# Kernel tuning notes

Hardware: AMD Instinct MI355X
Metric: run time of the kernel (lower is better)

Reference implementation:

```python
import jax, jax.numpy as jnp
import numpy as np

RADIUS = 0.15
NSAMPLE = 128
NPOINT = 128
EPS = 1e-5  # BatchNorm eps (eval mode, running_mean=0, running_var=1)


def _bn(x, g, b):
    shape = (1, -1) + (1,) * (x.ndim - 2)
    return x * (g / jnp.sqrt(1.0 + EPS)).reshape(shape) + b.reshape(shape)


def _fps(x, npoint):
    # farthest point sampling; x: (Bk, N, 3) -> (Bk, npoint) int32
    Bn, N, _ = x.shape

    def step(carry, _):
        dist, far = carry
        c = jnp.take_along_axis(x, far[:, None, None], 1)  # (Bk,1,3)
        d = jnp.sum((x - c) ** 2, -1)
        dist = jnp.minimum(dist, d)
        return (dist, jnp.argmax(dist, -1).astype(jnp.int32)), far

    init = (jnp.full((Bn, N), 1e10, x.dtype), jnp.zeros((Bn,), jnp.int32))
    _, idxs = jax.lax.scan(step, init, None, length=npoint)
    return idxs.T  # (Bk, npoint)


def _sa_module(x, f, mlp):
    # PointnetSAModuleVotes: FPS -> ball query -> group (use_xyz, normalize_xyz)
    # -> shared MLP (conv2d 1x1 + BN + ReLU) -> max over nsample.
    Bk, M, _ = x.shape
    fps_idx = _fps(x, NPOINT)
    new_xyz = jnp.take_along_axis(x, fps_idx[..., None], 1)  # (Bk,np,3)
    d2 = jnp.sum((new_xyz[:, :, None, :] - x[:, None, :, :]) ** 2, -1)  # (Bk,np,M)
    cand = jnp.where(d2 < RADIUS ** 2, jnp.arange(M)[None, None, :], M)
    cand = jnp.sort(cand, -1)[..., :NSAMPLE]  # first nsample in-radius indices
    first = cand[..., :1]
    first = jnp.where(first == M, 0, first)
    idx = jnp.where(cand == M, first, cand)  # (Bk,np,ns), pad with first valid
    gx = jnp.take_along_axis(x, idx.reshape(Bk, -1)[..., None], 1).reshape(Bk, NPOINT, NSAMPLE, 3)
    gxn = (gx - new_xyz[:, :, None, :]) / RADIUS  # normalize_xyz=True
    gf = jnp.take_along_axis(f[:, :, None, :], idx[:, None, :, :], 3)  # (Bk,C,np,ns)
    h = jnp.concatenate([gxn.transpose(0, 3, 1, 2), gf], 1)  # (Bk, C+3, np, ns)
    for (w, b, g, be) in mlp:
        h = jax.nn.relu(_bn(jnp.einsum('oc,bcps->bops', w, h) + b[None, :, None, None], g, be))
    return new_xyz, h.max(-1)  # (Bk,np,3), (Bk,128,np)


def setup_inputs() -> dict:
    key = jax.random.key(0)
    ks = iter(jax.random.split(key, 40))
    B, M, K, C = 2, 1024, 19, 256
    inp = {}
    inp['xyz'] = jax.random.normal(next(ks), (B, M, K, 3), jnp.float32)
    inp['features'] = jax.random.normal(next(ks), (B, C, K, M), jnp.float32)

    def conv_p(prefix, cin, cout):
        inp[prefix + '_w'] = jax.random.normal(next(ks), (cout, cin), jnp.float32) * (1.0 / np.sqrt(cin))
        inp[prefix + '_b'] = jax.random.normal(next(ks), (cout,), jnp.float32) * 0.02
        inp[prefix + '_g'] = 1.0 + 0.1 * jax.random.normal(next(ks), (cout,), jnp.float32)
        inp[prefix + '_be'] = 0.02 * jax.random.normal(next(ks), (cout,), jnp.float32)

    conv_p('m1', C + 3, 128)  # use_xyz -> 259 in-channels
    conv_p('m2', 128, 128)
    conv_p('m3', 128, 128)
    conv_p('c1', 128, 128)
    conv_p('c2', 128, 128)
    inp['op_w'] = jax.random.normal(next(ks), (K, 5, 128), jnp.float32) * (1.0 / np.sqrt(128))
    inp['op_b'] = jax.random.normal(next(ks), (K, 5), jnp.float32) * 0.02
    return inp


def reference(xyz, features, m1_w, m1_b, m1_g, m1_be, m2_w, m2_b, m2_g, m2_be,
              m3_w, m3_b, m3_g, m3_be, c1_w, c1_b, c1_g, c1_be,
              c2_w, c2_b, c2_g, c2_be, op_w, op_b):
    B, M, K, _ = xyz.shape
    C = features.shape[1]
    # fold vote_factor k into the batch dim (all per-k SA/conv weights are shared)
    x = xyz.transpose(0, 2, 1, 3).reshape(B * K, M, 3)
    f = features.transpose(0, 2, 1, 3).reshape(B * K, C, M)
    mlp = [(m1_w, m1_b, m1_g, m1_be), (m2_w, m2_b, m2_g, m2_be), (m3_w, m3_b, m3_g, m3_be)]
    new_xyz, feat = _sa_module(x, f, mlp)
    net = jax.nn.relu(_bn(jnp.einsum('oc,bcp->bop', c1_w, feat) + c1_b[None, :, None], c1_g, c1_be))
    net = jax.nn.relu(_bn(jnp.einsum('oc,bcp->bop', c2_w, net) + c2_b[None, :, None], c2_g, c2_be))
    net = net.reshape(B, K, 128, NPOINT)
    # per-k output conv (conv_op ModuleList), 128 -> 2+3
    out = jnp.einsum('koc,bkcp->bkop', op_w, net) + op_b[None, :, :, None]
    net_t = out.transpose(0, 1, 3, 2)  # (B,K,np,5)
    agg_xyz = new_xyz.reshape(B, K, NPOINT, 3)
    center = agg_xyz + net_t[..., 2:5]  # decode_scores_
    scores = jnp.concatenate([net_t[..., :2], center], -1)  # obj(2) + center(3)
    return scores, agg_xyz, feat.reshape(B, K, 128, NPOINT)
```

## Files before the change

kernel.cpp:

```cpp
#include <hip/hip_runtime.h>
#include <math.h>

#define NBK   38

#define OFF_XC    0u
#define OFF_NXYZ  466944u
#define OFF_BIDX  525312u
#define OFF_W1F   3015680u
#define OFF_PREP  22938624u
#define OFF_WF    22955008u
#define OFF_CNT   23348224u

#define OUT_AGG   24320
#define OUT_FEAT  38912

typedef short bf16x8 __attribute__((ext_vector_type(8)));
typedef float f32x4  __attribute__((ext_vector_type(4)));
typedef int   v4i    __attribute__((ext_vector_type(4)));
typedef int   v2i    __attribute__((ext_vector_type(2)));

__device__ __forceinline__ float dist2f(float a0, float a1, float a2,
                                        float b0, float b1, float b2) {
#pragma clang fp contract(off)
  float d0 = a0 - b0;
  float d1 = a1 - b1;
  float d2 = a2 - b2;
  return d0 * d0 + d1 * d1 + d2 * d2;
}

__device__ __forceinline__ void split2rn(float v, unsigned& sh, unsigned& sm) {
  unsigned u = __float_as_uint(v);
  unsigned rh = (u + 0x7fffu + ((u >> 16) & 1u)) & 0xffff0000u;
  sh = rh >> 16;
  float r1 = v - __uint_as_float(rh);
  unsigned u1 = __float_as_uint(r1);
  unsigned rm = (u1 + 0x7fffu + ((u1 >> 16) & 1u)) & 0xffff0000u;
  sm = rm >> 16;
}

#define DPP_FMAX_STEP(v, ctrl)                                                 \
  {                                                                            \
    int _s = __builtin_amdgcn_update_dpp(__float_as_int(v), __float_as_int(v), \
                                         (ctrl), 0xf, 0xf, false);             \
    (v) = fmaxf((v), __int_as_float(_s));                                      \
  }

__device__ __forceinline__ float readlane_f(float v, int l) {
  return __int_as_float(__builtin_amdgcn_readlane(__float_as_int(v), l));
}

__global__ __launch_bounds__(512, 2) void front_kernel(
    const float* __restrict__ xyz, const float* __restrict__ feats,
    const float* __restrict__ m1w, const float* __restrict__ m1b,
    const float* __restrict__ m1g, const float* __restrict__ m1be,
    const float* __restrict__ m2w, const float* __restrict__ m2b,
    const float* __restrict__ m2g, const float* __restrict__ m2be,
    const float* __restrict__ m3w, const float* __restrict__ m3b,
    const float* __restrict__ m3g, const float* __restrict__ m3be,
    const float* __restrict__ c1w, const float* __restrict__ c1b,
    const float* __restrict__ c1g, const float* __restrict__ c1be,
    const float* __restrict__ c2w, const float* __restrict__ c2b,
    const float* __restrict__ c2g, const float* __restrict__ c2be,
    float* __restrict__ xc, float* __restrict__ nxyz, float* __restrict__ agg,
    int* __restrict__ bidx, int* __restrict__ counts,
    float* __restrict__ W1f, short* __restrict__ Wf, float* __restrict__ prep)
{
  __shared__ __align__(16) char smem[32768];
  int bid = blockIdx.x, t = threadIdx.x;
  int wave = t >> 6, lane = t & 63;

  if (bid < NBK) {
    int bk = bid;
    int b = bk / 19, k = bk % 19;
    float4* sp4 = (float4*)smem;
    float4* scen4 = (float4*)(smem + 16384);
    int* sfar = (int*)(smem + 18432);
    int2* cexch = (int2*)(smem + 18944);

    for (int i = t; i < 1024; i += 512) {
      const float* src = xyz + ((size_t)((b * 1024 + i) * 19 + k)) * 3;
      float x0 = src[0], x1 = src[1], x2 = src[2];
      sp4[i] = make_float4(x0, x1, x2, 0.f);
      xc[(bk * 3 + 0) * 1024 + i] = x0;
      xc[(bk * 3 + 1) * 1024 + i] = x1;
      xc[(bk * 3 + 2) * 1024 + i] = x2;
    }
    if (t == 0) sfar[0] = 0;
    __syncthreads();

    float px[8], py[8], pz[8], dist[8];
    if (wave < 2) {
      __builtin_amdgcn_s_setprio(1);
      int mbase = (wave << 9) + (lane << 3);
#pragma unroll
      for (int j = 0; j < 8; ++j) {
        float4 p = sp4[mbase + j];
        px[j] = p.x; py[j] = p.y; pz[j] = p.z;
        dist[j] = 1e10f;
      }
    }

    int far = 0;
    for (int it = 1; it < 128; ++it) {
      if (wave < 2) {
        float4 c = sp4[far];
#pragma unroll
        for (int j = 0; j < 8; ++j) {
          float d = dist2f(px[j], py[j], pz[j], c.x, c.y, c.z);
          dist[j] = fminf(dist[j], d);
        }
        float tv[4]; int tj[4];
#pragma unroll
        for (int i = 0; i < 4; ++i) {
          bool L = dist[2 * i] >= dist[2 * i + 1];
          tv[i] = L ? dist[2 * i] : dist[2 * i + 1];
          tj[i] = L ? (2 * i) : (2 * i + 1);
        }
        {
          bool L0 = tv[0] >= tv[1];
          float v0 = L0 ? tv[0] : tv[1]; int j0 = L0 ? tj[0] : tj[1];
          bool L1 = tv[2] >= tv[3];
          float v1 = L1 ? tv[2] : tv[3]; int j1 = L1 ? tj[2] : tj[3];
          bool L = v0 >= v1;
          tv[0] = L ? v0 : v1; tj[0] = L ? j0 : j1;
        }
        float lmax = tv[0];
        float g = lmax;
        DPP_FMAX_STEP(g, 0x111);
        DPP_FMAX_STEP(g, 0x112);
        DPP_FMAX_STEP(g, 0x114);
        DPP_FMAX_STEP(g, 0x118);
        float r0 = readlane_f(g, 15);
        float r1 = readlane_f(g, 31);
        float r2 = readlane_f(g, 47);
        float r3 = readlane_f(g, 63);
        float gmax = fmaxf(fmaxf(r0, r1), fmaxf(r2, r3));
        unsigned long long mk = __ballot(lmax == gmax);
        int wl = (int)__builtin_ctzll(mk);
        int lj = (lane << 3) + tj[0];
        int cand_m = (wave << 9) + __builtin_amdgcn_readlane(lj, wl);
        if (lane == 0) cexch[(it & 1) * 2 + wave] =
            make_int2(__float_as_int(gmax), cand_m);
      }
      __syncthreads();
      if (wave < 2) {
        int2 c0 = cexch[(it & 1) * 2 + 0];
        int2 c1 = cexch[(it & 1) * 2 + 1];
        far = (__int_as_float(c1.x) > __int_as_float(c0.x)) ? c1.y : c0.y;
        if (t == 0) sfar[it] = far;
      }
    }
    if (wave < 2) __builtin_amdgcn_s_setprio(0);
    __syncthreads();

    if (t < 128) {
      float4 c = sp4[sfar[t]];
      scen4[t] = c;
      nxyz[bk * 384 + t * 3 + 0] = c.x;
      nxyz[bk * 384 + t * 3 + 1] = c.y;
      nxyz[bk * 384 + t * 3 + 2] = c.z;
      agg[bk * 384 + t * 3 + 0] = c.x;
      agg[bk * 384 + t * 3 + 1] = c.y;
      agg[bk * 384 + t * 3 + 2] = c.z;
    }
    __syncthreads();

    for (int p = wave * 16; p < wave * 16 + 16; ++p) {
      float4 cen = scen4[p];
      int* outp = bidx + ((size_t)(bk * 128 + p)) * 128;
      int count = 0, first = 0;
      bool got = false;
      for (int ch = 0; ch < 16 && count < 128; ++ch) {
        int m = (ch << 6) + lane;
        float4 pv = sp4[m];
        float d = dist2f(pv.x, pv.y, pv.z, cen.x, cen.y, cen.z);
        bool flag = d < 0.0225f;
        unsigned long long mask = __ballot(flag);
        if (!got && mask) { first = (ch << 6) + __builtin_ctzll(mask); got = true; }
        int pos = count + (int)__popcll(mask & ((1ull << lane) - 1ull));
        if (flag && pos < 128) outp[pos] = m;
        count += (int)__popcll(mask);
      }
      for (int j = count + lane; j < 128; j += 64) outp[j] = first;
      if (lane == 0) counts[bk * 128 + p] = count > 128 ? 128 : count;
    }
    return;
  }

  if (bid < 342) {
    short* ffrag = (short*)smem;
    if (t >= 256) {
      for (int i = 0; i < 8; ++i) __syncthreads();
      return;
    }
    int blk = bid - NBK;
    int bk = blk >> 3, m0 = (blk & 7) << 7;
    int b = bk / 19, k = bk % 19;
    int quad = lane >> 4, nl = lane & 15;
    int mloc = t & 127, chalf = t >> 7;
    int st_w = mloc >> 4, sl_w = mloc & 15;
    const float* fbase = feats + ((size_t)(b * 4864 + k)) * 1024 + m0 + mloc;

    f32x4 acc[2][8];
#pragma unroll
    for (int oi = 0; oi < 2; ++oi)
#pragma unroll
      for (int st = 0; st < 8; ++st) acc[oi][st] = (f32x4){0.f, 0.f, 0.f, 0.f};

    for (int ch = 0; ch < 4; ++ch) {
      int cbase = ch * 64 + chalf * 32;
#pragma unroll
      for (int g = 0; g < 4; ++g) {
        float v[8];
#pragma unroll
        for (int j = 0; j < 8; ++j)
          v[j] = fbase[(size_t)(cbase + g * 8 + j) * 19456];
        unsigned sh[8], sm[8];
#pragma unroll
        for (int j = 0; j < 8; ++j) split2rn(v[j], sh[j], sm[j]);
        int base = chalf * 4096 + st_w * 512 + (g * 16 + sl_w) * 8;
        v4i ph = {(int)(sh[0] | (sh[1] << 16)), (int)(sh[2] | (sh[3] << 16)),
                  (int)(sh[4] | (sh[5] << 16)), (int)(sh[6] | (sh[7] << 16))};
        *(v4i*)&ffrag[base] = ph;
        v4i pm = {(int)(sm[0] | (sm[1] << 16)), (int)(sm[2] | (sm[3] << 16)),
                  (int)(sm[4] | (sm[5] << 16)), (int)(sm[6] | (sm[7] << 16))};
        *(v4i*)&ffrag[base + 8192] = pm;
      }
      __syncthreads();
#pragma unroll
      for (int kkl = 0; kkl < 2; ++kkl) {
        int kk = ch * 2 + kkl;
        bf16x8 a[2][2];
#pragma unroll
        for (int oi = 0; oi < 2; ++oi) {
          int o_row = (wave * 2 + oi) * 16 + nl;
          const float* wsrc = m1w + o_row * 259 + 3 + kk * 32 + quad * 8;
          float wv[8];
#pragma unroll
          for (int j = 0; j < 8; ++j) wv[j] = wsrc[j];
          unsigned sh[8], sm[8];
#pragma unroll
          for (int j = 0; j < 8; ++j) split2rn(wv[j], sh[j], sm[j]);
          short ah[8], am[8];
#pragma unroll
          for (int j = 0; j < 8; ++j) { ah[j] = (short)sh[j]; am[j] = (short)sm[j]; }
          a[oi][0] = (bf16x8){ah[0], ah[1], ah[2], ah[3], ah[4], ah[5], ah[6], ah[7]};
          a[oi][1] = (bf16x8){am[0], am[1], am[2], am[3], am[4], am[5], am[6], am[7]};
        }
#pragma unroll
        for (int st = 0; st < 8; ++st) {
          const short* hb = ffrag + kkl * 4096 + st * 512 + lane * 8;
          bf16x8 b0 = *(const bf16x8*)hb;
          bf16x8 b1 = *(const bf16x8*)(hb + 8192);
#pragma unroll
          for (int oi = 0; oi < 2; ++oi) {
            f32x4 c = acc[oi][st];
            c = __builtin_amdgcn_mfma_f32_16x16x32_bf16(a[oi][1], b0, c, 0, 0, 0);
            c = __builtin_amdgcn_mfma_f32_16x16x32_bf16(a[oi][0], b1, c, 0, 0, 0);
            c = __builtin_amdgcn_mfma_f32_16x16x32_bf16(a[oi][0], b0, c, 0, 0, 0);
            acc[oi][st] = c;
          }
        }
      }
      __syncthreads();
    }
    float inv = 1.0f / sqrtf(1.0f + 1e-5f);
#pragma unroll
    for (int oi = 0; oi < 2; ++oi) {
      int o0 = (wave * 2 + oi) * 16 + quad * 4;
      float4 bb = *(const float4*)&m1b[o0];
      float4 gg = *(const float4*)&m1g[o0];
#pragma unroll
      for (int st = 0; st < 8; ++st) {
        int m_out = m0 + st * 16 + nl;
        f32x4 cc = acc[oi][st];
        float4 r;
        r.x = (cc[0] + bb.x) * (gg.x * inv);
        r.y = (cc[1] + bb.y) * (gg.y * inv);
        r.z = (cc[2] + bb.z) * (gg.z * inv);
        r.w = (cc[3] + bb.w) * (gg.w * inv);
        *(float4*)&W1f[((size_t)(bk * 1024 + m_out)) * 128 + o0] = r;
      }
    }
    return;
  }

  if (bid < 358) {
    int idx = (bid - 342) * 512 + t;
#pragma unroll
    for (int e = 0; e < 4; ++e) {
      int i = idx * 4 + e;
      int c = i & 127, o = (i >> 7) & 127, l = i >> 14;
      float w = (l ? m3w : m2w)[o * 128 + c];
      unsigned sh, sm;
      split2rn(w, sh, sm);
      int ot = o >> 4, mm = o & 15, kk = c >> 5, q = (c & 31) >> 3, j = c & 7;
      int within = (q * 16 + mm) * 8 + j;
      Wf[(((l * 2 + 0) * 4 + kk) * 8 + ot) * 512 + within] = (short)sh;
      Wf[(((l * 2 + 1) * 4 + kk) * 8 + ot) * 512 + within] = (short)sm;
    }
    return;
  }

  if (bid < 374) {
    int idx2 = (bid - 358) * 512 + t;
#pragma unroll
    for (int e = 0; e < 4; ++e) {
      int i = idx2 * 4 + e;
      int c = i & 127, o = (i >> 7) & 127, l = i >> 14;
      float w = (l ? c2w : c1w)[o * 128 + c];
      unsigned sh, sm;
      split2rn(w, sh, sm);
      int ot = o >> 4, mm = o & 15, kk = c >> 5, q = (c & 31) >> 3, j = c & 7;
      int within = (q * 16 + mm) * 8 + j;
      Wf[131072 + (((l * 2 + 0) * 4 + kk) * 8 + ot) * 512 + within] = (short)sh;
      Wf[131072 + (((l * 2 + 1) * 4 + kk) * 8 + ot) * 512 + within] = (short)sm;
    }
    return;
  }

  if (t < 128) {
    float inv = 1.0f / sqrtf(1.0f + 1e-5f);
    float a1 = m1g[t] * inv;
    prep[t] = a1;
    float a2 = m2g[t] * inv;  prep[256 + t] = a2;  prep[384 + t] = fmaf(m2b[t], a2, m2be[t]);
    float a3 = m3g[t] * inv;  prep[512 + t] = a3;  prep[640 + t] = fmaf(m3b[t], a3, m3be[t]);
    float ac1 = c1g[t] * inv; prep[768 + t] = ac1; prep[896 + t] = fmaf(c1b[t], ac1, c1be[t]);
    float ac2 = c2g[t] * inv; prep[1024 + t] = ac2; prep[1152 + t] = fmaf(c2b[t], ac2, c2be[t]);
    prep[1280 + 4 * t + 0] = m1w[t * 259 + 0] * a1;
    prep[1280 + 4 * t + 1] = m1w[t * 259 + 1] * a1;
    prep[1280 + 4 * t + 2] = m1w[t * 259 + 2] * a1;
    prep[1280 + 4 * t + 3] = m1be[t];
  }
}

__device__ __forceinline__ void mfma_layer(const short* __restrict__ Wf,
                                           const short* hfrag, int l,
                                           int wave, int lane, int nst_h,
                                           f32x4 acc[2][4])
{
#pragma unroll 1
  for (int kk = 0; kk < 4; ++kk) {
    bf16x8 a[2][2];
#pragma unroll
    for (int oi = 0; oi < 2; ++oi)
#pragma unroll
      for (int sp = 0; sp < 2; ++sp)
        a[oi][sp] = *(const bf16x8*)(Wf + (((l * 2 + sp) * 4 + kk) * 8 + (wave * 2 + oi)) * 512 + lane * 8);
    for (int st = 0; st < nst_h; ++st) {
      const short* hb = hfrag + kk * 2048 + st * 512 + lane * 8;
      bf16x8 b0 = *(const bf16x8*)(hb);
      bf16x8 b1 = *(const bf16x8*)(hb + 8192);
#pragma unroll
      for (int oi = 0; oi < 2; ++oi) {
        f32x4 c = acc[oi][st];
        c = __builtin_amdgcn_mfma_f32_16x16x32_bf16(a[oi][1], b0, c, 0, 0, 0);
        c = __builtin_amdgcn_mfma_f32_16x16x32_bf16(a[oi][0], b1, c, 0, 0, 0);
        c = __builtin_amdgcn_mfma_f32_16x16x32_bf16(a[oi][0], b0, c, 0, 0, 0);
        acc[oi][st] = c;
      }
    }
  }
}

__global__ __launch_bounds__(256, 3) void sa_kernel(
    const float* __restrict__ xc, const float* __restrict__ nxyz,
    const int* __restrict__ bidx, const int* __restrict__ counts,
    const float* __restrict__ W1f, const float* __restrict__ prep,
    const short* __restrict__ Wf, float* __restrict__ feat_out)
{
  __shared__ __align__(16) short hfrag[16384];
  __shared__ float pcs[512];
  __shared__ float sm[32 * 128];
  __shared__ float ccen[12];
  __shared__ int scnt[4];
  int gb = blockIdx.x, bk = gb >> 5, pb = (gb & 31) << 2;
  int t = threadIdx.x;
  int wave = t >> 6, lane = t & 63;
  int quad = lane >> 4, nl = lane & 15;

  pcs[t] = prep[1280 + t];
  pcs[256 + t] = prep[1536 + t];
  if (t < 4) scnt[t] = counts[bk * 128 + pb + t];
  if (t < 12) {
    int bb = t / 3, c = t % 3;
    ccen[t] = nxyz[(bk * 128 + pb + bb) * 3 + c];
  }
  __syncthreads();
  int n0 = (scnt[0] + 15) >> 4, n1 = (scnt[1] + 15) >> 4;
  int n2 = (scnt[2] + 15) >> 4, n3 = (scnt[3] + 15) >> 4;
  int pf1 = n0, pf2 = n0 + n1, pf3 = n0 + n1 + n2, T = n0 + n1 + n2 + n3;

  for (int q0 = 0; q0 < T; q0 += 4) {
    int nst_h = T - q0;
    if (nst_h > 4) nst_h = 4;
    {
      int cg = wave;
      int st = lane >> 4, sl = lane & 15;
      if (st < nst_h) {
        int q = q0 + st;
        int bq = (q >= pf1) + (q >= pf2) + (q >= pf3);
        int tstart = (bq == 0) ? 0 : (bq == 1) ? pf1 : (bq == 2) ? pf2 : pf3;
        int tslot = q - tstart;
        int m = bidx[((size_t)(bk * 128 + pb + bq)) * 128 + tslot * 16 + sl];
        float cen0 = ccen[bq * 3 + 0], cen1 = ccen[bq * 3 + 1], cen2 = ccen[bq * 3 + 2];
        float g0 = (xc[(bk * 3 + 0) * 1024 + m] - cen0) * (1.0f / 0.15f);
        float g1 = (xc[(bk * 3 + 1) * 1024 + m] - cen1) * (1.0f / 0.15f);
        float g2 = (xc[(bk * 3 + 2) * 1024 + m] - cen2) * (1.0f / 0.15f);
        const float4* wrow = (const float4*)(W1f + ((size_t)(bk * 1024 + m)) * 128 + cg * 32);
        const float4* pcp = (const float4*)pcs + cg * 32;
#pragma unroll
        for (int g = 0; g < 4; ++g) {
          float4 wva = wrow[g * 2], wvb = wrow[g * 2 + 1];
          float wv[8] = {wva.x, wva.y, wva.z, wva.w, wvb.x, wvb.y, wvb.z, wvb.w};
          unsigned sh[8], smv[8];
#pragma unroll
          for (int e = 0; e < 8; ++e) {
            float4 pc = pcp[g * 8 + e];
            float hv = fmaxf(wv[e] + pc.x * g0 + pc.y * g1 + pc.z * g2 + pc.w, 0.f);
            split2rn(hv, sh[e], smv[e]);
          }
          int base = (cg * 4 + st) * 512 + (g * 16 + sl) * 8;
          v4i ph = {(int)(sh[0] | (sh[1] << 16)), (int)(sh[2] | (sh[3] << 16)),
                    (int)(sh[4] | (sh[5] << 16)), (int)(sh[6] | (sh[7] << 16))};
          *(v4i*)&hfrag[base] = ph;
          v4i pm = {(int)(smv[0] | (smv[1] << 16)), (int)(smv[2] | (smv[3] << 16)),
                    (int)(smv[4] | (smv[5] << 16)), (int)(smv[6] | (smv[7] << 16))};
          *(v4i*)&hfrag[base + 8192] = pm;
        }
      }
    }
    __syncthreads();

    f32x4 acc[2][4];
#pragma unroll
    for (int oi = 0; oi < 2; ++oi)
#pragma unroll
      for (int st = 0; st < 4; ++st) acc[oi][st] = (f32x4){0.f, 0.f, 0.f, 0.f};
    mfma_layer(Wf, hfrag, 0, wave, lane, nst_h, acc);
    __syncthreads();

#pragma unroll
    for (int oi = 0; oi < 2; ++oi) {
      int o0 = (wave * 2 + oi) * 16 + quad * 4;
      float4 al = *(const float4*)&prep[256 + o0];
      float4 be = *(const float4*)&prep[384 + o0];
      int kk2 = o0 >> 5, g2 = (o0 & 31) >> 3, j0 = o0 & 7;
      for (int st = 0; st < nst_h; ++st) {
        f32x4 cc = acc[oi][st];
        float v0 = fmaxf(fmaf(cc[0], al.x, be.x), 0.f);
        float v1 = fmaxf(fmaf(cc[1], al.y, be.y), 0.f);
        float v2 = fmaxf(fmaf(cc[2], al.z, be.z), 0.f);
        float v3 = fmaxf(fmaf(cc[3], al.w, be.w), 0.f);
        unsigned h0, m0_, h1, m1_, h2, m2_, h3, m3_;
        split2rn(v0, h0, m0_); split2rn(v1, h1, m1_);
        split2rn(v2, h2, m2_); split2rn(v3, h3, m3_);
        int base = (kk2 * 4 + st) * 512 + (g2 * 16 + nl) * 8 + j0;
        v2i w0 = {(int)(h0 | (h1 << 16)), (int)(h2 | (h3 << 16))};
        *(v2i*)&hfrag[base] = w0;
        v2i w1 = {(int)(m0_ | (m1_ << 16)), (int)(m2_ | (m3_ << 16))};
        *(v2i*)&hfrag[base + 8192] = w1;
      }
    }
    __syncthreads();

#pragma unroll
    for (int oi = 0; oi < 2; ++oi)
#pragma unroll
      for (int st = 0; st < 4; ++st) acc[oi][st] = (f32x4){0.f, 0.f, 0.f, 0.f};
    mfma_layer(Wf, hfrag, 1, wave, lane, nst_h, acc);

#pragma unroll
    for (int oi = 0; oi < 2; ++oi) {
      int o0 = (wave * 2 + oi) * 16 + quad * 4;
      float4 al = *(const float4*)&prep[512 + o0];
      float4 be = *(const float4*)&prep[640 + o0];
      for (int st = 0; st < nst_h; ++st) {
        f32x4 cc = acc[oi][st];
        float v[4];
        v[0] = fmaxf(fmaf(cc[0], al.x, be.x), 0.f);
        v[1] = fmaxf(fmaf(cc[1], al.y, be.y), 0.f);
        v[2] = fmaxf(fmaf(cc[2], al.z, be.z), 0.f);
        v[3] = fmaxf(fmaf(cc[3], al.w, be.w), 0.f);
#pragma unroll
        for (int r = 0; r < 4; ++r) {
          float x = v[r];
          x = fmaxf(x, __shfl_xor(x, 1));
          x = fmaxf(x, __shfl_xor(x, 2));
          x = fmaxf(x, __shfl_xor(x, 4));
          x = fmaxf(x, __shfl_xor(x, 8));
          if (nl == 0) sm[(q0 + st) * 128 + o0 + r] = x;
        }
      }
    }
    __syncthreads();
  }

#pragma unroll
  for (int e = t; e < 512; e += 256) {
    int bb = e >> 7, o = e & 127;
    int qs = (bb == 0) ? 0 : (bb == 1) ? pf1 : (bb == 2) ? pf2 : pf3;
    int nq = (bb == 0) ? n0 : (bb == 1) ? n1 : (bb == 2) ? n2 : n3;
    float v = sm[qs * 128 + o];
    for (int q = 1; q < nq; ++q) v = fmaxf(v, sm[(qs + q) * 128 + o]);
    feat_out[(((size_t)bk) << 14) + (o << 7) + pb + bb] = v;
  }
}

__global__ __launch_bounds__(256) void head_kernel(const float* __restrict__ featg,
    const float* __restrict__ prep, const short* __restrict__ Wf,
    const float* __restrict__ nxyz, const float* __restrict__ opw,
    const float* __restrict__ opb, float* __restrict__ scores)
{
  __shared__ __align__(16) short hfrag[16384];
  __shared__ float hplain[128 * 65];
  int bk = blockIdx.x >> 1, p0 = (blockIdx.x & 1) << 6;
  int t = threadIdx.x;
  int wave = t >> 6, lane = t & 63;
  int quad = lane >> 4, nl = lane & 15;
  const short* WC = Wf + 131072;

  {
    int cg = wave;
    int st = lane >> 4, sl = lane & 15;
    const float* fb = featg + (bk << 14) + p0 + lane;
#pragma unroll
    for (int g = 0; g < 4; ++g) {
      float v[8];
#pragma unroll
      for (int e = 0; e < 8; ++e)
        v[e] = fb[(cg * 32 + g * 8 + e) << 7];
      unsigned sh[8], sm[8];
#pragma unroll
      for (int e = 0; e < 8; ++e) split2rn(v[e], sh[e], sm[e]);
      int base = (cg * 4 + st) * 512 + (g * 16 + sl) * 8;
      v4i ph = {(int)(sh[0] | (sh[1] << 16)), (int)(sh[2] | (sh[3] << 16)),
                (int)(sh[4] | (sh[5] << 16)), (int)(sh[6] | (sh[7] << 16))};
      *(v4i*)&hfrag[base] = ph;
      v4i pm = {(int)(sm[0] | (sm[1] << 16)), (int)(sm[2] | (sm[3] << 16)),
                (int)(sm[4] | (sm[5] << 16)), (int)(sm[6] | (sm[7] << 16))};
      *(v4i*)&hfrag[base + 8192] = pm;
    }
  }
  __syncthreads();

  f32x4 acc[2][4];
#pragma unroll
  for (int oi = 0; oi < 2; ++oi)
#pragma unroll
    for (int st = 0; st < 4; ++st) acc[oi][st] = (f32x4){0.f, 0.f, 0.f, 0.f};
  mfma_layer(WC, hfrag, 0, wave, lane, 4, acc);
  __syncthreads();

#pragma unroll
  for (int oi = 0; oi < 2; ++oi) {
    int o0 = (wave * 2 + oi) * 16 + quad * 4;
    float4 al = *(const float4*)&prep[768 + o0];
    float4 be = *(const float4*)&prep[896 + o0];
    int kk2 = o0 >> 5, g2 = (o0 & 31) >> 3, j0 = o0 & 7;
#pragma unroll
    for (int st = 0; st < 4; ++st) {
      f32x4 cc = acc[oi][st];
      float v0 = fmaxf(fmaf(cc[0], al.x, be.x), 0.f);
      float v1 = fmaxf(fmaf(cc[1], al.y, be.y), 0.f);
      float v2 = fmaxf(fmaf(cc[2], al.z, be.z), 0.f);
      float v3 = fmaxf(fmaf(cc[3], al.w, be.w), 0.f);
      unsigned h0, m0_, h1, m1_, h2, m2_, h3, m3_;
      split2rn(v0, h0, m0_); split2rn(v1, h1, m1_);
      split2rn(v2, h2, m2_); split2rn(v3, h3, m3_);
      int base = (kk2 * 4 + st) * 512 + (g2 * 16 + nl) * 8 + j0;
      v2i w0 = {(int)(h0 | (h1 << 16)), (int)(h2 | (h3 << 16))};
      *(v2i*)&hfrag[base] = w0;
      v2i w1 = {(int)(m0_ | (m1_ << 16)), (int)(m2_ | (m3_ << 16))};
      *(v2i*)&hfrag[base + 8192] = w1;
    }
  }
  __syncthreads();

#pragma unroll
  for (int oi = 0; oi < 2; ++oi)
#pragma unroll
    for (int st = 0; st < 4; ++st) acc[oi][st] = (f32x4){0.f, 0.f, 0.f, 0.f};
  mfma_layer(WC, hfrag, 1, wave, lane, 4, acc);

#pragma unroll
  for (int oi = 0; oi < 2; ++oi) {
    int o0 = (wave * 2 + oi) * 16 + quad * 4;
    float4 al = *(const float4*)&prep[1024 + o0];
    float4 be = *(const float4*)&prep[1152 + o0];
#pragma unroll
    for (int st = 0; st < 4; ++st) {
      f32x4 cc = acc[oi][st];
      int p = st * 16 + nl;
      hplain[(o0 + 0) * 65 + p] = fmaxf(fmaf(cc[0], al.x, be.x), 0.f);
      hplain[(o0 + 1) * 65 + p] = fmaxf(fmaf(cc[1], al.y, be.y), 0.f);
      hplain[(o0 + 2) * 65 + p] = fmaxf(fmaf(cc[2], al.z, be.z), 0.f);
      hplain[(o0 + 3) * 65 + p] = fmaxf(fmaf(cc[3], al.w, be.w), 0.f);
    }
  }
  __syncthreads();

  if (t < 64) {
    int p = t, k = bk % 19;
    float res[5];
#pragma unroll
    for (int j = 0; j < 5; ++j) {
      const float* wr = opw + ((size_t)(k * 5 + j)) * 128;
      float a = opb[k * 5 + j];
      for (int c = 0; c < 128; ++c) a = fmaf(wr[c], hplain[c * 65 + p], a);
      res[j] = a;
    }
    int pg = p0 + p;
    float a0 = nxyz[(bk * 128 + pg) * 3 + 0];
    float a1 = nxyz[(bk * 128 + pg) * 3 + 1];
    float a2 = nxyz[(bk * 128 + pg) * 3 + 2];
    float* sc = scores + ((size_t)(bk * 128 + pg)) * 5;
    sc[0] = res[0];
    sc[1] = res[1];
    sc[2] = a0 + res[2];
    sc[3] = a1 + res[3];
    sc[4] = a2 + res[4];
  }
}

extern "C" void kernel_launch(void* const* d_in, const int* in_sizes, int n_in,
                              void* d_out, int out_size, void* d_ws, size_t ws_size,
                              hipStream_t stream) {
  (void)in_sizes; (void)n_in; (void)out_size; (void)ws_size;
  const float* xyz  = (const float*)d_in[0];
  const float* fts  = (const float*)d_in[1];
  const float* m1w  = (const float*)d_in[2];
  const float* m1b  = (const float*)d_in[3];
  const float* m1g  = (const float*)d_in[4];
  const float* m1be = (const float*)d_in[5];
  const float* m2w  = (const float*)d_in[6];
  const float* m2b  = (const float*)d_in[7];
  const float* m2g  = (const float*)d_in[8];
  const float* m2be = (const float*)d_in[9];
  const float* m3w  = (const float*)d_in[10];
  const float* m3b  = (const float*)d_in[11];
  const float* m3g  = (const float*)d_in[12];
  const float* m3be = (const float*)d_in[13];
  const float* c1w  = (const float*)d_in[14];
  const float* c1b  = (const float*)d_in[15];
  const float* c1g  = (const float*)d_in[16];
  const float* c1be = (const float*)d_in[17];
  const float* c2w  = (const float*)d_in[18];
  const float* c2b  = (const float*)d_in[19];
  const float* c2g  = (const float*)d_in[20];
  const float* c2be = (const float*)d_in[21];
  const float* opw  = (const float*)d_in[22];
  const float* opb  = (const float*)d_in[23];

  float* out = (float*)d_out;
  char* ws = (char*)d_ws;
  float* xc   = (float*)(ws + OFF_XC);
  float* nxyz = (float*)(ws + OFF_NXYZ);
  int*   bidx = (int*)(ws + OFF_BIDX);
  float* W1f  = (float*)(ws + OFF_W1F);
  float* prep = (float*)(ws + OFF_PREP);
  short* Wf   = (short*)(ws + OFF_WF);
  int*   cnt  = (int*)(ws + OFF_CNT);

  hipLaunchKernelGGL(front_kernel, dim3(375), dim3(512), 0, stream,
                     xyz, fts, m1w, m1b, m1g, m1be, m2w, m2b, m2g, m2be,
                     m3w, m3b, m3g, m3be, c1w, c1b, c1g, c1be,
                     c2w, c2b, c2g, c2be,
                     xc, nxyz, out + OUT_AGG, bidx, cnt, W1f, Wf, prep);
  hipLaunchKernelGGL(sa_kernel, dim3(NBK * 32), dim3(256), 0, stream,
                     xc, nxyz, bidx, cnt, W1f, prep, Wf, out + OUT_FEAT);
  hipLaunchKernelGGL(head_kernel, dim3(NBK * 2), dim3(256), 0, stream,
                     out + OUT_FEAT, prep, Wf, nxyz, opw, opb, out);
}
```

Before: 284.4 us.

## Use all 512 threads in layer-1 feature GEMM blocks, halve block count

The layer-1 feature projection blocks previously idled half their threads (t>=256 just waited on barriers). Now all 8 waves participate: each wave computes 16 output channels instead of 32, the feature staging is split across four thread groups, and each block processes two 128-point halves sequentially, cutting the front grid from 375 to 223 blocks. This aims to raise per-block utilization and reduce idle threads, at the cost of less parallelism per block output and more serialized work per block.

```diff
diff --git a/kernel.cpp b/kernel.cpp
--- a/kernel.cpp
+++ b/kernel.cpp
@@ -187,93 +187,86 @@
     return;
   }
 
-  if (bid < 342) {
+  if (bid < 190) {
     short* ffrag = (short*)smem;
-    if (t >= 256) {
-      for (int i = 0; i < 8; ++i) __syncthreads();
-      return;
-    }
     int blk = bid - NBK;
-    int bk = blk >> 3, m0 = (blk & 7) << 7;
+    int bk = blk >> 2, mq = blk & 3;
     int b = bk / 19, k = bk % 19;
     int quad = lane >> 4, nl = lane & 15;
-    int mloc = t & 127, chalf = t >> 7;
+    int mloc = t & 127, cq = t >> 7;
+    int chalf = cq >> 1, ghalf = cq & 1;
     int st_w = mloc >> 4, sl_w = mloc & 15;
-    const float* fbase = feats + ((size_t)(b * 4864 + k)) * 1024 + m0 + mloc;
-
-    f32x4 acc[2][8];
-#pragma unroll
-    for (int oi = 0; oi < 2; ++oi)
-#pragma unroll
-      for (int st = 0; st < 8; ++st) acc[oi][st] = (f32x4){0.f, 0.f, 0.f, 0.f};
-
-    for (int ch = 0; ch < 4; ++ch) {
-      int cbase = ch * 64 + chalf * 32;
-#pragma unroll
-      for (int g = 0; g < 4; ++g) {
-        float v[8];
-#pragma unroll
-        for (int j = 0; j < 8; ++j)
-          v[j] = fbase[(size_t)(cbase + g * 8 + j) * 19456];
-        unsigned sh[8], sm[8];
-#pragma unroll
-        for (int j = 0; j < 8; ++j) split2rn(v[j], sh[j], sm[j]);
-        int base = chalf * 4096 + st_w * 512 + (g * 16 + sl_w) * 8;
-        v4i ph = {(int)(sh[0] | (sh[1] << 16)), (int)(sh[2] | (sh[3] << 16)),
-                  (int)(sh[4] | (sh[5] << 16)), (int)(sh[6] | (sh[7] << 16))};
-        *(v4i*)&ffrag[base] = ph;
-        v4i pm = {(int)(sm[0] | (sm[1] << 16)), (int)(sm[2] | (sm[3] << 16)),
-                  (int)(sm[4] | (sm[5] << 16)), (int)(sm[6] | (sm[7] << 16))};
-        *(v4i*)&ffrag[base + 8192] = pm;
-      }
-      __syncthreads();
-#pragma unroll
-      for (int kkl = 0; kkl < 2; ++kkl) {
-        int kk = ch * 2 + kkl;
-        bf16x8 a[2][2];
-#pragma unroll
-        for (int oi = 0; oi < 2; ++oi) {
-          int o_row = (wave * 2 + oi) * 16 + nl;
-          const float* wsrc = m1w + o_row * 259 + 3 + kk * 32 + quad * 8;
-          float wv[8];
-#pragma unroll
-          for (int j = 0; j < 8; ++j) wv[j] = wsrc[j];
+
+    for (int half = 0; half < 2; ++half) {
+      int m0 = (mq << 8) + (half << 7);
+      const float* fbase = feats + ((size_t)(b * 4864 + k)) * 1024 + m0 + mloc;
+
+      f32x4 acc[8];
+#pragma unroll
+      for (int st = 0; st < 8; ++st) acc[st] = (f32x4){0.f, 0.f, 0.f, 0.f};
+
+      for (int ch = 0; ch < 4; ++ch) {
+        int cbase = ch * 64 + chalf * 32;
+#pragma unroll
+        for (int g2 = 0; g2 < 2; ++g2) {
+          int g = ghalf * 2 + g2;
+          float v[8];
+#pragma unroll
+          for (int j = 0; j < 8; ++j)
+            v[j] = fbase[(size_t)(cbase + g * 8 + j) * 19456];
           unsigned sh[8], sm[8];
 #pragma unroll
-          for (int j = 0; j < 8; ++j) split2rn(wv[j], sh[j], sm[j]);
-          short ah[8], am[8];
-#pragma unroll
-          for (int j = 0; j < 8; ++j) { ah[j] = (short)sh[j]; am[j] = (short)sm[j]; }
-          a[oi][0] = (bf16x8){ah[0], ah[1], ah[2], ah[3], ah[4], ah[5], ah[6], ah[7]};
-          a[oi][1] = (bf16x8){am[0], am[1], am[2], am[3], am[4], am[5], am[6], am[7]};
+          for (int j = 0; j < 8; ++j) split2rn(v[j], sh[j], sm[j]);
+          int base = chalf * 4096 + st_w * 512 + (g * 16 + sl_w) * 8;
+          v4i ph = {(int)(sh[0] | (sh[1] << 16)), (int)(sh[2] | (sh[3] << 16)),
+                    (int)(sh[4] | (sh[5] << 16)), (int)(sh[6] | (sh[7] << 16))};
+          *(v4i*)&ffrag[base] = ph;
+          v4i pm = {(int)(sm[0] | (sm[1] << 16)), (int)(sm[2] | (sm[3] << 16)),
+                    (int)(sm[4] | (sm[5] << 16)), (int)(sm[6] | (sm[7] << 16))};
+          *(v4i*)&ffrag[base + 8192] = pm;
         }
-#pragma unroll
-        for (int st = 0; st < 8; ++st) {
-          const short* hb = ffrag + kkl * 4096 + st * 512 + lane * 8;
-          bf16x8 b0 = *(const bf16x8*)hb;
-          bf16x8 b1 = *(const bf16x8*)(hb + 8192);
-#pragma unroll
-          for (int oi = 0; oi < 2; ++oi) {
-            f32x4 c = acc[oi][st];
-            c = __builtin_amdgcn_mfma_f32_16x16x32_bf16(a[oi][1], b0, c, 0, 0, 0);
-            c = __builtin_amdgcn_mfma_f32_16x16x32_bf16(a[oi][0], b1, c, 0, 0, 0);
-            c = __builtin_amdgcn_mfma_f32_16x16x32_bf16(a[oi][0], b0, c, 0, 0, 0);
-            acc[oi][st] = c;
+        __syncthreads();
+#pragma unroll
+        for (int kkl = 0; kkl < 2; ++kkl) {
+          int kk = ch * 2 + kkl;
+          bf16x8 a0, a1;
+          {
+            int o_row = wave * 16 + nl;
+            const float* wsrc = m1w + o_row * 259 + 3 + kk * 32 + quad * 8;
+            float wv[8];
+#pragma unroll
+            for (int j = 0; j < 8; ++j) wv[j] = wsrc[j];
+            unsigned sh[8], sm[8];
+#pragma unroll
+            for (int j = 0; j < 8; ++j) split2rn(wv[j], sh[j], sm[j]);
+            short ah[8], am[8];
+#pragma unroll
+            for (int j = 0; j < 8; ++j) { ah[j] = (short)sh[j]; am[j] = (short)sm[j]; }
+            a0 = (bf16x8){ah[0], ah[1], ah[2], ah[3], ah[4], ah[5], ah[6], ah[7]};
+            a1 = (bf16x8){am[0], am[1], am[2], am[3], am[4], am[5], am[6], am[7]};
+          }
+#pragma unroll
+          for (int st = 0; st < 8; ++st) {
+            const short* hb = ffrag + kkl * 4096 + st * 512 + lane * 8;
+            bf16x8 b0 = *(const bf16x8*)hb;
+            bf16x8 b1 = *(const bf16x8*)(hb + 8192);
+            f32x4 c = acc[st];
+            c = __builtin_amdgcn_mfma_f32_16x16x32_bf16(a1, b0, c, 0, 0, 0);
+            c = __builtin_amdgcn_mfma_f32_16x16x32_bf16(a0, b1, c, 0, 0, 0);
+            c = __builtin_amdgcn_mfma_f32_16x16x32_bf16(a0, b0, c, 0, 0, 0);
+            acc[st] = c;
           }
         }
-      }
-      __syncthreads();
-    }
-    float inv = 1.0f / sqrtf(1.0f + 1e-5f);
-#pragma unroll
-    for (int oi = 0; oi < 2; ++oi) {
-      int o0 = (wave * 2 + oi) * 16 + quad * 4;
+        __syncthreads();
+      }
+      float inv = 1.0f / sqrtf(1.0f + 1e-5f);
+      int o0 = wave * 16 + quad * 4;
       float4 bb = *(const float4*)&m1b[o0];
       float4 gg = *(const float4*)&m1g[o0];
 #pragma unroll
       for (int st = 0; st < 8; ++st) {
         int m_out = m0 + st * 16 + nl;
-        f32x4 cc = acc[oi][st];
+        f32x4 cc = acc[st];
         float4 r;
         r.x = (cc[0] + bb.x) * (gg.x * inv);
         r.y = (cc[1] + bb.y) * (gg.y * inv);
@@ -285,8 +278,8 @@
     return;
   }
 
-  if (bid < 358) {
-    int idx = (bid - 342) * 512 + t;
+  if (bid < 206) {
+    int idx = (bid - 190) * 512 + t;
 #pragma unroll
     for (int e = 0; e < 4; ++e) {
       int i = idx * 4 + e;
@@ -302,8 +295,8 @@
     return;
   }
 
-  if (bid < 374) {
-    int idx2 = (bid - 358) * 512 + t;
+  if (bid < 222) {
+    int idx2 = (bid - 206) * 512 + t;
 #pragma unroll
     for (int e = 0; e < 4; ++e) {
       int i = idx2 * 4 + e;
@@ -662,7 +655,7 @@
   short* Wf   = (short*)(ws + OFF_WF);
   int*   cnt  = (int*)(ws + OFF_CNT);
 
-  hipLaunchKernelGGL(front_kernel, dim3(375), dim3(512), 0, stream,
+  hipLaunchKernelGGL(front_kernel, dim3(223), dim3(512), 0, stream,
                      xyz, fts, m1w, m1b, m1g, m1be, m2w, m2b, m2g, m2be,
                      m3w, m3b, m3g, m3be, c1w, c1b, c1g, c1be,
                      c2w, c2b, c2g, c2be,
```

After: 283.8 us. No clear change (-0.2%).
